# Performance work log

Hardware: AMD Instinct MI355X
Metric: run time of the kernel (lower is better)

The kernel has to match this reference:

```python
import jax, jax.numpy as jnp
import numpy as np

N_HEADS = 16
N_KV_HEADS = 4
HEAD_DIM = 128
NEG_INF = -1e9


def setup_inputs() -> dict:
    key = jax.random.key(0)
    ks = jax.random.split(key, 6)
    bs, seq, d_model = 2, 2048, 2048
    x = jax.random.normal(ks[0], (bs, seq, d_model), jnp.float32)
    # RoPE table: theta = 10000^{-2i/head_dim}, angle = pos * theta
    inv_freq = 1.0 / (10000.0 ** (jnp.arange(0, HEAD_DIM, 2, dtype=jnp.float32) / HEAD_DIM))
    ang = jnp.arange(seq, dtype=jnp.float32)[:, None] * inv_freq[None, :]  # [seq, head_dim/2]
    freqs_cos = jnp.cos(ang)
    freqs_sin = jnp.sin(ang)
    # causal additive mask
    mask = jnp.where(jnp.tril(jnp.ones((seq, seq), dtype=bool)), 0.0, NEG_INF).astype(jnp.float32)
    s = 1.0 / np.sqrt(d_model)
    wq = jax.random.normal(ks[1], (d_model, N_HEADS * HEAD_DIM), jnp.float32) * s
    wk = jax.random.normal(ks[2], (d_model, N_KV_HEADS * HEAD_DIM), jnp.float32) * s
    wv = jax.random.normal(ks[3], (d_model, N_KV_HEADS * HEAD_DIM), jnp.float32) * s
    wo = jax.random.normal(ks[4], (N_HEADS * HEAD_DIM, d_model), jnp.float32) * s
    return {"x": x, "freqs_cos": freqs_cos, "freqs_sin": freqs_sin, "mask": mask,
            "wq": wq, "wk": wk, "wv": wv, "wo": wo}


def _rope(t, cos, sin):
    # t: [b, h, s, d]; cos/sin: [s, d/2]
    b, h, s, d = t.shape
    tp = t.reshape(b, h, s, d // 2, 2)
    x0, x1 = tp[..., 0], tp[..., 1]
    c = cos[None, None, :, :]
    sn = sin[None, None, :, :]
    o0 = x0 * c - x1 * sn
    o1 = x0 * sn + x1 * c
    return jnp.stack([o0, o1], axis=-1).reshape(b, h, s, d)


def reference(x, freqs_cos, freqs_sin, mask, wq, wk, wv, wo):
    bs, seq, d_model = x.shape
    rep = N_HEADS // N_KV_HEADS
    q = (x @ wq).reshape(bs, seq, N_HEADS, HEAD_DIM).transpose(0, 2, 1, 3)
    k = (x @ wk).reshape(bs, seq, N_KV_HEADS, HEAD_DIM).transpose(0, 2, 1, 3)
    v = (x @ wv).reshape(bs, seq, N_KV_HEADS, HEAD_DIM).transpose(0, 2, 1, 3)
    q = _rope(q, freqs_cos, freqs_sin)
    k = _rope(k, freqs_cos, freqs_sin)
    # GQA: group q heads over kv heads instead of materially repeating kv
    qg = q.reshape(bs, N_KV_HEADS, rep, seq, HEAD_DIM)
    scores = jnp.einsum('bgrsd,bgtd->bgrst', qg, k) / np.sqrt(HEAD_DIM)
    scores = scores + mask[None, None, None, :, :]
    attn = jax.nn.softmax(scores, axis=-1)
    out = jnp.einsum('bgrst,bgtd->bgrsd', attn, v)
    out = out.reshape(bs, N_HEADS, seq, HEAD_DIM).transpose(0, 2, 1, 3).reshape(bs, seq, -1)
    return out @ wo
```

## Files before the change

kernel.cpp:

```cpp
#include <hip/hip_runtime.h>
#include <hip/hip_bf16.h>

#define SEQ 2048
#define DM 2048
#define NH 16
#define NKV 4
#define HD 128

typedef float f32x4 __attribute__((ext_vector_type(4)));
typedef short s16x8 __attribute__((ext_vector_type(8)));
typedef short s16x4 __attribute__((ext_vector_type(4)));

__device__ inline __hip_bfloat16 f2b(float f) { return __float2bfloat16(f); }
__device__ inline float b2f_us(unsigned short u) { return __uint_as_float(((unsigned)u) << 16); }
__device__ inline short f2b_s(float f) {
    __hip_bfloat16 h = __float2bfloat16(f);
    return *(short*)&h;
}

__device__ inline void gl_lds16(const void* g, void* l) {
    __builtin_amdgcn_global_load_lds((const __attribute__((address_space(1))) void*)g,
                                     (__attribute__((address_space(3))) void*)l, 16, 0, 0);
}

__global__ void cast_kernel(const float* __restrict__ in, __hip_bfloat16* __restrict__ out, int n) {
    int i = (blockIdx.x * 256 + threadIdx.x) * 4;
    if (i < n) {
        float4 v = *(const float4*)(in + i);
        __hip_bfloat16 o4[4] = {f2b(v.x), f2b(v.y), f2b(v.z), f2b(v.w)};
        *(ushort4*)(out + i) = *(ushort4*)o4;
    }
}

__global__ void transpose_cast(const float* __restrict__ in, __hip_bfloat16* __restrict__ out,
                               int K, int N) {
    __shared__ float tile[32][33];
    int n0 = blockIdx.x * 32, k0 = blockIdx.y * 32;
    int tx = threadIdx.x, ty = threadIdx.y;
    for (int r = ty; r < 32; r += 8)
        tile[r][tx] = in[(size_t)(k0 + r) * N + n0 + tx];
    __syncthreads();
    for (int r = ty; r < 32; r += 8)
        out[(size_t)(n0 + r) * K + k0 + tx] = f2b(tile[tx][r]);
}

template <int OUT_F32>
__global__ __launch_bounds__(256, 3) void gemm_bt(
    const __hip_bfloat16* __restrict__ A,
    const __hip_bfloat16* __restrict__ Bt,
    void* __restrict__ Cp, int M, int N, int Kd) {
    __shared__ __hip_bfloat16 As[128 * 64];
    __shared__ __hip_bfloat16 Bs[128 * 64];
    const int nx = gridDim.x, ny = gridDim.y;
    const int pid = blockIdx.y * nx + blockIdx.x;
    const int GM = 8;
    const int grp = pid / (GM * nx);
    const int first = grp * GM;
    const int gsz = (ny - first < GM) ? (ny - first) : GM;
    const int mt = first + (pid % gsz);
    const int ntile = (pid % (GM * nx)) / gsz;
    const int m0 = mt * 128, n0 = ntile * 128;

    const int t = threadIdx.x;
    const int wv = t >> 6, lane = t & 63;
    const int wm = (wv >> 1) * 64, wn = (wv & 1) * 64;
    const int lrow = lane & 15, quad = lane >> 4;
    f32x4 acc[4][4];
    f32x4 z4 = {0.f, 0.f, 0.f, 0.f};
    for (int i = 0; i < 4; ++i)
        for (int j = 0; j < 4; ++j) acc[i][j] = z4;

    for (int k0 = 0; k0 < Kd; k0 += 64) {
        __syncthreads();
        for (int i = 0; i < 4; ++i) {
            int flat = i * 256 + t;
            int row = flat >> 3;
            int cb = (flat & 7) ^ (row & 7);
            gl_lds16(A + (size_t)(m0 + row) * Kd + k0 + cb * 8, &As[flat * 8]);
            gl_lds16(Bt + (size_t)(n0 + row) * Kd + k0 + cb * 8, &Bs[flat * 8]);
        }
        __syncthreads();
        for (int kk = 0; kk < 2; ++kk) {
            s16x8 af[4], bf[4];
            for (int i = 0; i < 4; ++i) {
                int ra = wm + i * 16 + lrow;
                int rb = wn + i * 16 + lrow;
                int pba = ((kk * 4 + quad) ^ (ra & 7)) * 8;
                int pbb = ((kk * 4 + quad) ^ (rb & 7)) * 8;
                af[i] = *(const s16x8*)&As[ra * 64 + pba];
                bf[i] = *(const s16x8*)&Bs[rb * 64 + pbb];
            }
            for (int i = 0; i < 4; ++i)
                for (int j = 0; j < 4; ++j)
                    acc[i][j] = __builtin_amdgcn_mfma_f32_16x16x32_bf16(af[i], bf[j],
                                                                        acc[i][j], 0, 0, 0);
        }
    }
    for (int i = 0; i < 4; ++i)
        for (int j = 0; j < 4; ++j)
            for (int r = 0; r < 4; ++r) {
                int m = m0 + wm + i * 16 + quad * 4 + r;
                int n = n0 + wn + j * 16 + lrow;
                if (OUT_F32)
                    ((float*)Cp)[(size_t)m * N + n] = acc[i][j][r];
                else
                    ((__hip_bfloat16*)Cp)[(size_t)m * N + n] = f2b(acc[i][j][r]);
            }
}

__global__ void rope_reshape(const __hip_bfloat16* __restrict__ qkv,
                             const float* __restrict__ fcos, const float* __restrict__ fsin,
                             __hip_bfloat16* __restrict__ q, __hip_bfloat16* __restrict__ k) {
    int tok = blockIdx.x;
    int b = tok >> 11, s = tok & 2047;
    const __hip_bfloat16* row = qkv + (size_t)tok * 3072;
    for (int it = threadIdx.x; it < 320; it += 256) {
        int col = it * 8;
        s16x8 v = *(const s16x8*)(row + col);
        int p0 = (col & 127) >> 1;
        f32x4 c4 = *(const f32x4*)(fcos + s * 64 + p0);
        f32x4 s4 = *(const f32x4*)(fsin + s * 64 + p0);
        short outv[8];
        for (int p = 0; p < 4; ++p) {
            float x0 = b2f_us((unsigned short)v[2 * p]);
            float x1 = b2f_us((unsigned short)v[2 * p + 1]);
            outv[2 * p] = f2b_s(x0 * c4[p] - x1 * s4[p]);
            outv[2 * p + 1] = f2b_s(x0 * s4[p] + x1 * c4[p]);
        }
        int d = col & 127;
        if (col < 2048) {
            int h = col >> 7;
            *(s16x8*)(q + ((size_t)((b * NH + h) * SEQ + s)) * HD + d) = *(s16x8*)outv;
        } else {
            int h = (col - 2048) >> 7;
            *(s16x8*)(k + ((size_t)((b * NKV + h) * SEQ + s)) * HD + d) = *(s16x8*)outv;
        }
    }
}

__global__ void vtrans(const __hip_bfloat16* __restrict__ qkv, __hip_bfloat16* __restrict__ vt) {
    __shared__ __hip_bfloat16 tile[128][136];
    int s0 = blockIdx.x * 128;
    int bh = blockIdx.y;
    int b = bh >> 2, kvh = bh & 3;
    int t = threadIdx.x;
    for (int i = 0; i < 8; ++i) {
        int flat = (i * 256 + t) * 8;
        int row = flat >> 7, col = flat & 127;
        *(s16x8*)&tile[row][col] =
            *(const s16x8*)(qkv + (size_t)(b * SEQ + s0 + row) * 3072 + 2560 + kvh * 128 + col);
    }
    __syncthreads();
    for (int i = 0; i < 8; ++i) {
        int dd = i * 16 + (t >> 4);
        int ss = (t & 15) * 8;
        __hip_bfloat16 tmp[8];
        for (int j = 0; j < 8; ++j) tmp[j] = tile[ss + j][dd];
        *(s16x8*)(vt + ((size_t)((b * NKV + kvh) * HD + dd)) * SEQ + s0 + ss) = *(s16x8*)tmp;
    }
}

__global__ __launch_bounds__(512, 4) void attn_kernel(
    const __hip_bfloat16* __restrict__ q, const __hip_bfloat16* __restrict__ k,
    const __hip_bfloat16* __restrict__ vt, __hip_bfloat16* __restrict__ o) {
    __shared__ __hip_bfloat16 Ks[64][136];
    __shared__ __hip_bfloat16 Vs[128][72];
    __shared__ __hip_bfloat16 Ps[8][16][72];

    const int bh = blockIdx.y;
    const int bx = (bh < 16) ? (int)(gridDim.x - 1 - blockIdx.x) : (int)blockIdx.x;
    const int b = bh >> 4, h = bh & 15;
    const int kvh = h >> 2;
    const int t = threadIdx.x;
    const int w = t >> 6, lane = t & 63;
    const int lrow = lane & 15, quad = lane >> 4;
    const int q0 = bx * 128;
    const int qrow = q0 + w * 16 + lrow;
    const float scale = 0.08838834764831845f;

    const __hip_bfloat16* qp = q + ((size_t)((b * NH + h) * SEQ + qrow)) * HD;
    s16x8 qf[4];
    for (int ks = 0; ks < 4; ++ks) qf[ks] = *(const s16x8*)(qp + ks * 32 + quad * 8);

    float m_i = -1e30f, l_i = 0.f;
    f32x4 accO[8];
    f32x4 z4 = {0.f, 0.f, 0.f, 0.f};
    for (int d = 0; d < 8; ++d) accO[d] = z4;

    const __hip_bfloat16* kbase = k + ((size_t)(b * NKV + kvh) * SEQ) * HD;
    const __hip_bfloat16* vbase = vt + ((size_t)(b * NKV + kvh) * HD) * SEQ;

    s16x8 kr[2], vr[2];
    auto load_tile = [&](int kt) {
        for (int i = 0; i < 2; ++i) {
            int flat = (i * 512 + t) * 8;
            kr[i] = *(const s16x8*)(kbase + (size_t)(kt * 64 + (flat >> 7)) * HD + (flat & 127));
            vr[i] = *(const s16x8*)(vbase + (size_t)(flat >> 6) * SEQ + kt * 64 + (flat & 63));
        }
    };
    auto store_tile = [&]() {
        for (int i = 0; i < 2; ++i) {
            int flat = (i * 512 + t) * 8;
            *(s16x8*)&Ks[flat >> 7][flat & 127] = kr[i];
            *(s16x8*)&Vs[flat >> 6][flat & 63] = vr[i];
        }
    };

    const int nkt = 2 * bx + 2;
    load_tile(0);
    store_tile();
    __syncthreads();

    for (int kt = 0; kt < nkt; ++kt) {
        bool more = (kt + 1) < nkt;
        if (more) load_tile(kt + 1);
        bool wave_active = (kt * 64 <= q0 + w * 16 + 15);
        bool mtile = (kt >= 2 * bx);

        if (wave_active) {
            float sv[4][4];
            for (int nt = 0; nt < 4; ++nt) {
                f32x4 sacc = z4;
                for (int ks = 0; ks < 4; ++ks) {
                    s16x8 kf = *(const s16x8*)&Ks[nt * 16 + lrow][ks * 32 + quad * 8];
                    sacc = __builtin_amdgcn_mfma_f32_16x16x32_bf16(kf, qf[ks], sacc, 0, 0, 0);
                }
                for (int r = 0; r < 4; ++r) {
                    int key = kt * 64 + nt * 16 + quad * 4 + r;
                    sv[nt][r] = (mtile && key > qrow) ? -1e30f : sacc[r] * scale;
                }
            }
            float mt2 = -1e30f;
            for (int nt = 0; nt < 4; ++nt)
                for (int r = 0; r < 4; ++r) mt2 = fmaxf(mt2, sv[nt][r]);
            mt2 = fmaxf(mt2, __shfl_xor(mt2, 16, 64));
            mt2 = fmaxf(mt2, __shfl_xor(mt2, 32, 64));
            float mn = fmaxf(m_i, mt2);
            float alpha = __expf(m_i - mn);
            m_i = mn;
            float rs = 0.f;
            for (int nt = 0; nt < 4; ++nt) {
                short ph[4];
                for (int r = 0; r < 4; ++r) {
                    float p = __expf(sv[nt][r] - mn);
                    rs += p;
                    ph[r] = f2b_s(p);
                }
                *(s16x4*)&Ps[w][lrow][nt * 16 + quad * 4] = *(s16x4*)ph;
            }
            rs += __shfl_xor(rs, 16, 64);
            rs += __shfl_xor(rs, 32, 64);
            l_i = l_i * alpha + rs;
            for (int d = 0; d < 8; ++d)
                for (int r = 0; r < 4; ++r) accO[d][r] *= alpha;
            s16x8 pf0 = *(const s16x8*)&Ps[w][lrow][quad * 8];
            s16x8 pf1 = *(const s16x8*)&Ps[w][lrow][32 + quad * 8];
            for (int dt = 0; dt < 8; ++dt) {
                s16x8 vf0 = *(const s16x8*)&Vs[dt * 16 + lrow][quad * 8];
                s16x8 vf1 = *(const s16x8*)&Vs[dt * 16 + lrow][32 + quad * 8];
                accO[dt] = __builtin_amdgcn_mfma_f32_16x16x32_bf16(vf0, pf0, accO[dt], 0, 0, 0);
                accO[dt] = __builtin_amdgcn_mfma_f32_16x16x32_bf16(vf1, pf1, accO[dt], 0, 0, 0);
            }
        }

        __syncthreads();
        if (more) {
            store_tile();
            __syncthreads();
        }
    }
    float inv = 1.0f / l_i;
    __hip_bfloat16* op = o + (size_t)(b * SEQ + qrow) * DM + h * HD;
    for (int dt = 0; dt < 8; ++dt) {
        short ov[4];
        for (int r = 0; r < 4; ++r) ov[r] = f2b_s(accO[dt][r] * inv);
        *(s16x4*)(op + dt * 16 + quad * 4) = *(s16x4*)ov;
    }
}

extern "C" void kernel_launch(void* const* d_in, const int* in_sizes, int n_in,
                              void* d_out, int out_size, void* d_ws, size_t ws_size,
                              hipStream_t stream) {
    (void)in_sizes; (void)n_in; (void)out_size; (void)ws_size;
    const float* x  = (const float*)d_in[0];
    const float* fc = (const float*)d_in[1];
    const float* fs = (const float*)d_in[2];
    const float* wq = (const float*)d_in[4];
    const float* wk = (const float*)d_in[5];
    const float* wv = (const float*)d_in[6];
    const float* wo = (const float*)d_in[7];

    __hip_bfloat16* xb    = (__hip_bfloat16*)d_ws;
    __hip_bfloat16* wqkvt = xb + (size_t)8388608;
    __hip_bfloat16* wot   = wqkvt + (size_t)6291456;
    __hip_bfloat16* qkv   = wot + (size_t)4194304;
    __hip_bfloat16* qb    = xb;
    __hip_bfloat16* kb    = wqkvt;
    __hip_bfloat16* vtb   = wqkvt + (size_t)2097152;
    __hip_bfloat16* attno = qkv;

    cast_kernel<<<8192, 256, 0, stream>>>(x, xb, 8388608);
    transpose_cast<<<dim3(64, 64), dim3(32, 8), 0, stream>>>(wq, wqkvt, 2048, 2048);
    transpose_cast<<<dim3(16, 64), dim3(32, 8), 0, stream>>>(wk, wqkvt + (size_t)2048 * 2048, 2048, 512);
    transpose_cast<<<dim3(16, 64), dim3(32, 8), 0, stream>>>(wv, wqkvt + (size_t)2560 * 2048, 2048, 512);
    transpose_cast<<<dim3(64, 64), dim3(32, 8), 0, stream>>>(wo, wot, 2048, 2048);
    gemm_bt<0><<<dim3(24, 32), 256, 0, stream>>>(xb, wqkvt, qkv, 4096, 3072, 2048);
    rope_reshape<<<4096, 256, 0, stream>>>(qkv, fc, fs, qb, kb);
    vtrans<<<dim3(16, 8), 256, 0, stream>>>(qkv, vtb);
    attn_kernel<<<dim3(16, 32), 512, 0, stream>>>(qb, kb, vtb, attno);
    gemm_bt<1><<<dim3(16, 32), 256, 0, stream>>>(attno, wot, d_out, 4096, 2048, 2048);
}
```

Baseline: 334.1 us.

## Double-buffer K/V tiles in LDS and keep P in registers via permuted V layout

Makes the K and V shared-memory tiles double-buffered, so each iteration needs one barrier instead of two and the next tile is stored while other waves may still be computing. It also drops the per-wave P staging buffer in LDS. Softmax probabilities are packed straight into MFMA operand registers, and V is written to LDS in a permuted key order that matches the register layout of P. This saves an LDS round trip and a write-read dependency per tile. The cost is more LDS per block, which may lower occupancy, and a more intricate index permutation that must be exactly right.

```diff
diff --git a/kernel.cpp b/kernel.cpp
--- a/kernel.cpp
+++ b/kernel.cpp
@@ -163,9 +163,8 @@
 __global__ __launch_bounds__(512, 4) void attn_kernel(
     const __hip_bfloat16* __restrict__ q, const __hip_bfloat16* __restrict__ k,
     const __hip_bfloat16* __restrict__ vt, __hip_bfloat16* __restrict__ o) {
-    __shared__ __hip_bfloat16 Ks[64][136];
-    __shared__ __hip_bfloat16 Vs[128][72];
-    __shared__ __hip_bfloat16 Ps[8][16][72];
+    __shared__ __hip_bfloat16 Ks[2][64][136];
+    __shared__ __hip_bfloat16 Vs[2][128][72];
 
     const int bh = blockIdx.y;
     const int bx = (bh < 16) ? (int)(gridDim.x - 1 - blockIdx.x) : (int)blockIdx.x;
@@ -198,21 +197,27 @@
             vr[i] = *(const s16x8*)(vbase + (size_t)(flat >> 6) * SEQ + kt * 64 + (flat & 63));
         }
     };
-    auto store_tile = [&]() {
+    auto store_tile = [&](int bsel) {
         for (int i = 0; i < 2; ++i) {
             int flat = (i * 512 + t) * 8;
-            *(s16x8*)&Ks[flat >> 7][flat & 127] = kr[i];
-            *(s16x8*)&Vs[flat >> 6][flat & 63] = vr[i];
+            *(s16x8*)&Ks[bsel][flat >> 7][flat & 127] = kr[i];
+            int row = flat >> 6, k0 = flat & 63;
+            int pb = ((k0 >> 5) << 5) | (((k0 >> 2) & 2) << 3) | (((k0 >> 4) & 1) << 2);
+            s16x4 lo = {vr[i][0], vr[i][1], vr[i][2], vr[i][3]};
+            s16x4 hi = {vr[i][4], vr[i][5], vr[i][6], vr[i][7]};
+            *(s16x4*)&Vs[bsel][row][pb] = lo;
+            *(s16x4*)&Vs[bsel][row][pb + 8] = hi;
         }
     };
 
     const int nkt = 2 * bx + 2;
     load_tile(0);
-    store_tile();
-    __syncthreads();
+    store_tile(0);
 
     for (int kt = 0; kt < nkt; ++kt) {
+        const int cur = kt & 1;
         bool more = (kt + 1) < nkt;
+        __syncthreads();
         if (more) load_tile(kt + 1);
         bool wave_active = (kt * 64 <= q0 + w * 16 + 15);
         bool mtile = (kt >= 2 * bx);
@@ -222,7 +227,7 @@
             for (int nt = 0; nt < 4; ++nt) {
                 f32x4 sacc = z4;
                 for (int ks = 0; ks < 4; ++ks) {
-                    s16x8 kf = *(const s16x8*)&Ks[nt * 16 + lrow][ks * 32 + quad * 8];
+                    s16x8 kf = *(const s16x8*)&Ks[cur][nt * 16 + lrow][ks * 32 + quad * 8];
                     sacc = __builtin_amdgcn_mfma_f32_16x16x32_bf16(kf, qf[ks], sacc, 0, 0, 0);
                 }
                 for (int r = 0; r < 4; ++r) {
@@ -239,35 +244,29 @@
             float alpha = __expf(m_i - mn);
             m_i = mn;
             float rs = 0.f;
-            for (int nt = 0; nt < 4; ++nt) {
-                short ph[4];
-                for (int r = 0; r < 4; ++r) {
-                    float p = __expf(sv[nt][r] - mn);
-                    rs += p;
-                    ph[r] = f2b_s(p);
-                }
-                *(s16x4*)&Ps[w][lrow][nt * 16 + quad * 4] = *(s16x4*)ph;
+            s16x8 pf0, pf1;
+#pragma unroll
+            for (int j = 0; j < 8; ++j) {
+                float p0 = __expf(sv[j >> 2][j & 3] - mn);
+                float p1 = __expf(sv[2 + (j >> 2)][j & 3] - mn);
+                rs += p0 + p1;
+                pf0[j] = f2b_s(p0);
+                pf1[j] = f2b_s(p1);
             }
             rs += __shfl_xor(rs, 16, 64);
             rs += __shfl_xor(rs, 32, 64);
             l_i = l_i * alpha + rs;
             for (int d = 0; d < 8; ++d)
                 for (int r = 0; r < 4; ++r) accO[d][r] *= alpha;
-            s16x8 pf0 = *(const s16x8*)&Ps[w][lrow][quad * 8];
-            s16x8 pf1 = *(const s16x8*)&Ps[w][lrow][32 + quad * 8];
             for (int dt = 0; dt < 8; ++dt) {
-                s16x8 vf0 = *(const s16x8*)&Vs[dt * 16 + lrow][quad * 8];
-                s16x8 vf1 = *(const s16x8*)&Vs[dt * 16 + lrow][32 + quad * 8];
+                s16x8 vf0 = *(const s16x8*)&Vs[cur][dt * 16 + lrow][quad * 8];
+                s16x8 vf1 = *(const s16x8*)&Vs[cur][dt * 16 + lrow][32 + quad * 8];
                 accO[dt] = __builtin_amdgcn_mfma_f32_16x16x32_bf16(vf0, pf0, accO[dt], 0, 0, 0);
                 accO[dt] = __builtin_amdgcn_mfma_f32_16x16x32_bf16(vf1, pf1, accO[dt], 0, 0, 0);
             }
         }
 
-        __syncthreads();
-        if (more) {
-            store_tile();
-            __syncthreads();
-        }
+        if (more) store_tile(1 - cur);
     }
     float inv = 1.0f / l_i;
     __hip_bfloat16* op = o + (size_t)(b * SEQ + qrow) * DM + h * HD;
```

Result: no change. 335.6 us (+0.4%).
